# Kernel tuning notes

Measured on AMD Instinct MI355X. Metric: run time of the kernel, lower is better.

The kernel has to match this reference:

```python
import jax, jax.numpy as jnp
import numpy as np

B, T, V, E, H = 4096, 16, 512, 512, 1024


def setup_inputs() -> dict:
    key = jax.random.key(0)
    ks = jax.random.split(key, 8)
    s = 0.05  # weight init scale
    return {
        "encoded_input": jax.random.normal(ks[0], (B, H), jnp.float32),
        "target": jax.random.randint(ks[1], (B, T), 0, V, jnp.int32),
        "emb": jax.random.normal(ks[2], (V, E), jnp.float32) * s,
        "W_ih": jax.random.normal(ks[3], (4 * H, E), jnp.float32) * s,
        "W_hh": jax.random.normal(ks[4], (4 * H, H), jnp.float32) * s,
        "b_ih": jax.random.normal(ks[5], (4 * H,), jnp.float32) * s,
        "b_hh": jax.random.normal(ks[6], (4 * H,), jnp.float32) * s,
        "W_out": jax.random.normal(ks[7], (V, H), jnp.float32) * s,
    }


def reference(encoded_input, target, emb, W_ih, W_hh, b_ih, b_hh, W_out):
    # Teacher-forced char LSTM decoder. Dropout(0.1) is identity in eval mode.
    b, t = target.shape
    # input char ids: start token 0, then shifted targets
    inp_ids = jnp.concatenate(
        [jnp.zeros((b, 1), target.dtype), target[:, :-1]], axis=1)  # [B,T]
    x = emb[inp_ids]  # [B,T,E]
    # precompute input contribution to gates for all steps
    xg = jnp.einsum('bte,ge->btg', x, W_ih) + b_ih + b_hh  # [B,T,4H]

    def step(carry, xs):
        h, c = carry
        xg_t, tgt_t = xs  # [B,4H], [B]
        gates = xg_t + h @ W_hh.T  # [B,4H]
        i, f, g, o = jnp.split(gates, 4, axis=-1)  # torch order i,f,g,o
        i = jax.nn.sigmoid(i)
        f = jax.nn.sigmoid(f)
        g = jnp.tanh(g)
        o = jax.nn.sigmoid(o)
        c = f * c + i * g
        h = o * jnp.tanh(c)
        logits = h @ W_out.T  # [B,V]
        # NLL of log_softmax at target index, expressed stably
        lse = jax.nn.logsumexp(logits, axis=-1)
        tgt_logit = jnp.take_along_axis(logits, tgt_t[:, None], axis=1)[:, 0]
        loss_t = lse - tgt_logit  # [B]
        return (h, c), loss_t

    h0 = encoded_input  # hidden = (encoded, encoded) for 1 layer
    (_, _), losses = jax.lax.scan(
        step, (h0, h0),
        (jnp.swapaxes(xg, 0, 1), target.T))  # scan over time: [T,B,...]
    return losses.sum(axis=0) / t  # [B] per-example mean loss
```

## Files before the change

### kernel.cpp

```cpp
#include <hip/hip_runtime.h>
#include <hip/hip_bf16.h>
#include <stdint.h>

typedef __attribute__((ext_vector_type(8))) short bf16x8;
typedef __attribute__((ext_vector_type(4))) float f32x4;

#define DEV __device__ __forceinline__
#define MFMA16(a, b, c) __builtin_amdgcn_mfma_f32_16x16x32_bf16(a, b, c, 0, 0, 0)

static constexpr int Bn = 4096;
static constexpr int Tn = 16;
static constexpr int Vn = 512;
static constexpr int En = 512;
static constexpr int Hn = 1024;
static constexpr int G4 = 4096;

DEV unsigned short f2bf(float f) {
    union { float f; uint32_t u; } v; v.f = f;
    return (unsigned short)((v.u + 0x7fffu + ((v.u >> 16) & 1u)) >> 16);
}
DEV float bf2f(unsigned short h) {
    union { uint32_t u; float f; } v; v.u = (uint32_t)h << 16; return v.f;
}
DEV float sigmoidf_(float x) { return 1.f / (1.f + __expf(-x)); }
DEV float tanhf_(float x)    { return 1.f - 2.f / (1.f + __expf(2.f * x)); }

DEV bf16x8 cvt8(const float* p) {
    f32x4 a = *(const f32x4*)p;
    f32x4 b = *(const f32x4*)(p + 4);
    bf16x8 o;
    o[0] = (short)f2bf(a[0]); o[1] = (short)f2bf(a[1]);
    o[2] = (short)f2bf(a[2]); o[3] = (short)f2bf(a[3]);
    o[4] = (short)f2bf(b[0]); o[5] = (short)f2bf(b[1]);
    o[6] = (short)f2bf(b[2]); o[7] = (short)f2bf(b[3]);
    return o;
}

#define GLOAD16(s, d) __builtin_amdgcn_global_load_lds( \
    (const __attribute__((address_space(1))) uint32_t*)(s), \
    (__attribute__((address_space(3))) uint32_t*)(d), 16, 0, 0)

__launch_bounds__(1024, 4)
__global__ void lstm8(const unsigned short* __restrict__ Whp8,
                      const unsigned short* __restrict__ Hin,
                      const unsigned short* __restrict__ EGb,
                      const int* __restrict__ target, int t,
                      unsigned short* __restrict__ CstF,
                      unsigned short* __restrict__ Hout)
{
    __shared__ __align__(16) unsigned short lds[65536];

    const int tid = threadIdx.x;
    const int l   = tid & 63;
    const int w   = tid >> 6;
    const int wm  = w >> 2, wn = w & 3;
    const int q   = l >> 4, c15 = l & 15;
    const int bx  = blockIdx.x, by = blockIdx.y;
    const int n0  = bx * 256;
    const int U0  = by * 64;

    const int cBt = (((tid & 7) ^ ((tid >> 3) & 7)) << 3);
    const int sw0   = ((q ^ (c15 & 7)) << 3);
    const int offA0 = wm * 4096 + c15 * 64 + sw0;
    const int offB0 = wn * 4096 + c15 * 64 + sw0;

    f32x4 acc[4][4];
#pragma unroll
    for (int i = 0; i < 4; i++)
#pragma unroll
        for (int j = 0; j < 4; j++) acc[i][j] = f32x4{0.f, 0.f, 0.f, 0.f};

    auto stA = [&](int kts, int cbuf) {
        const unsigned short* page =
            Whp8 + (((size_t)(by * 16 + kts) * 2) << 13);
#pragma unroll
        for (int h = 0; h < 2; h++)
            GLOAD16(page + h * 8192 + tid * 8,
                    &lds[cbuf * 16384 + h * 8192 + tid * 8]);
    };
    auto stB = [&](int kts, int cbuf) {
#pragma unroll
        for (int h = 0; h < 2; h++)
            GLOAD16(Hin + (size_t)(n0 + h * 128 + (tid >> 3)) * Hn
                        + kts * 64 + cBt,
                    &lds[32768 + cbuf * 16384 + h * 8192 + tid * 8]);
    };

    stA(0, 0); stB(0, 0);
    stA(1, 1); stB(1, 1);
    asm volatile("s_waitcnt vmcnt(4)" ::: "memory");
    __builtin_amdgcn_s_barrier();

#pragma unroll 2
    for (int kt = 0; kt < 16; kt++) {
        const int cur = kt & 1;
        const unsigned short* Ab = &lds[cur * 16384];
        const unsigned short* Bb = &lds[32768 + cur * 16384];
        bf16x8 aF[4], bF[4];

#pragma unroll
        for (int i = 0; i < 4; i++)
            aF[i] = *(const bf16x8*)&Ab[offA0 + i * 1024];
#pragma unroll
        for (int j = 0; j < 4; j++)
            bF[j] = *(const bf16x8*)&Bb[offB0 + j * 1024];
        __builtin_amdgcn_s_setprio(1);
#pragma unroll
        for (int i = 0; i < 4; i++)
#pragma unroll
            for (int j = 0; j < 4; j++)
                acc[i][j] = MFMA16(aF[i], bF[j], acc[i][j]);
        __builtin_amdgcn_s_setprio(0);

#pragma unroll
        for (int i = 0; i < 4; i++)
            aF[i] = *(const bf16x8*)&Ab[(offA0 ^ 32) + i * 1024];
#pragma unroll
        for (int j = 0; j < 4; j++)
            bF[j] = *(const bf16x8*)&Bb[(offB0 ^ 32) + j * 1024];
        __builtin_amdgcn_s_setprio(1);
#pragma unroll
        for (int i = 0; i < 4; i++)
#pragma unroll
            for (int j = 0; j < 4; j++)
                acc[i][j] = MFMA16(aF[i], bF[j], acc[i][j]);
        __builtin_amdgcn_s_setprio(0);
        __builtin_amdgcn_s_barrier();

        const int kts = (kt + 2 < 16) ? (kt + 2) : 15;
        stA(kts, cur);
        stB(kts, cur);
        asm volatile("s_waitcnt vmcnt(4)" ::: "memory");
        __builtin_amdgcn_s_barrier();
    }

    int ids[4];
#pragma unroll
    for (int j = 0; j < 4; j++)
        ids[j] = (t > 0)
            ? target[(size_t)(n0 + wn * 64 + j * 16 + c15) * Tn + (t - 1)] : 0;

    unsigned short* sH = &lds[32768];
#pragma unroll
    for (int i = 0; i < 4; i++) {
        const int Uloc = wm * 16 + i * 4 + q;
#pragma unroll
        for (int j = 0; j < 4; j++) {
            uint2 egu = *(const uint2*)&EGb[(size_t)ids[j] * G4 + (U0 + Uloc) * 4];
            float e0 = bf2f((unsigned short)(egu.x & 0xffffu));
            float e1 = bf2f((unsigned short)(egu.x >> 16));
            float e2 = bf2f((unsigned short)(egu.y & 0xffffu));
            float e3 = bf2f((unsigned short)(egu.y >> 16));
            float ig = sigmoidf_(acc[i][j][0] + e0);
            float fg = sigmoidf_(acc[i][j][1] + e1);
            float gg = tanhf_  (acc[i][j][2] + e2);
            float og = sigmoidf_(acc[i][j][3] + e3);
            const size_t cidx =
                ((((size_t)(by * 16 + bx) * 16 + w) * 16 + i * 4 + j) << 6) + l;
            float cOld = bf2f(CstF[cidx]);
            float cNew = fg * cOld + ig * gg;
            float h    = og * tanhf_(cNew);
            CstF[cidx] = f2bf(cNew);
            const int bl = wn * 64 + j * 16 + c15;
            sH[bl * 64 + (Uloc ^ ((bl & 7) << 3))] = f2bf(h);
        }
    }
    __syncthreads();
    {
        const int row  = tid >> 2;
        const int part = tid & 3;
        size_t go = (size_t)(n0 + row) * Hn + U0;
#pragma unroll
        for (int s = 0; s < 2; s++) {
            const int slog = part * 2 + s;
            bf16x8 v = *(const bf16x8*)&sH[row * 64 + ((slog ^ (row & 7)) << 3)];
            *(bf16x8*)&Hout[go + slog * 8] = v;
        }
    }
}

__launch_bounds__(1024, 4)
__global__ void logits256(const unsigned short* __restrict__ A,
                          const unsigned short* __restrict__ Wob,
                          const int* __restrict__ target,
                          float* __restrict__ partS,
                          float* __restrict__ partT)
{
    __shared__ __align__(16) unsigned short lds[65536];
    __shared__ float redS[4 * 256];
    __shared__ float redT[4 * 256];
    __shared__ int   tgL[256];

    const int tid = threadIdx.x;
    const int l   = tid & 63;
    const int w   = tid >> 6;
    const int wm  = w >> 2, wn = w & 3;
    const int q   = l >> 4, c15 = l & 15;
    const int bid = blockIdx.x;
    const int rb  = bid & 255, cb = bid >> 8;
    const int r0  = rb * 256;
    const int v0  = cb * 256;

    if (tid < 256) {
        int ra = r0 + tid;
        tgL[tid] = target[(size_t)(ra & (Bn - 1)) * Tn + (ra >> 12)];
    }

    const int cBt = (((tid & 7) ^ ((tid >> 3) & 7)) << 3);
    const int sw0   = ((q ^ (c15 & 7)) << 3);
    const int offA0 = wm * 4096 + c15 * 64 + sw0;
    const int offB0 = wn * 4096 + c15 * 64 + sw0;

    f32x4 acc[4][4];
#pragma unroll
    for (int i = 0; i < 4; i++)
#pragma unroll
        for (int j = 0; j < 4; j++) acc[i][j] = f32x4{0.f, 0.f, 0.f, 0.f};

    auto stA = [&](int kts, int cbuf) {
#pragma unroll
        for (int h = 0; h < 2; h++)
            GLOAD16(A + (size_t)(r0 + h * 128 + (tid >> 3)) * Hn
                        + kts * 64 + cBt,
                    &lds[cbuf * 16384 + h * 8192 + tid * 8]);
    };
    auto stB = [&](int kts, int cbuf) {
#pragma unroll
        for (int h = 0; h < 2; h++)
            GLOAD16(Wob + (size_t)(v0 + h * 128 + (tid >> 3)) * Hn
                        + kts * 64 + cBt,
                    &lds[32768 + cbuf * 16384 + h * 8192 + tid * 8]);
    };

    stA(0, 0); stB(0, 0);
    stA(1, 1); stB(1, 1);
    asm volatile("s_waitcnt vmcnt(4)" ::: "memory");
    __builtin_amdgcn_s_barrier();

#pragma unroll 2
    for (int kt = 0; kt < 16; kt++) {
        const int cur = kt & 1;
        const unsigned short* Ab = &lds[cur * 16384];
        const unsigned short* Bb = &lds[32768 + cur * 16384];
        bf16x8 aF[4], bF[4];

#pragma unroll
        for (int i = 0; i < 4; i++)
            aF[i] = *(const bf16x8*)&Ab[offA0 + i * 1024];
#pragma unroll
        for (int j = 0; j < 4; j++)
            bF[j] = *(const bf16x8*)&Bb[offB0 + j * 1024];
        __builtin_amdgcn_s_setprio(1);
#pragma unroll
        for (int i = 0; i < 4; i++)
#pragma unroll
            for (int j = 0; j < 4; j++)
                acc[i][j] = MFMA16(aF[i], bF[j], acc[i][j]);
        __builtin_amdgcn_s_setprio(0);

#pragma unroll
        for (int i = 0; i < 4; i++)
            aF[i] = *(const bf16x8*)&Ab[(offA0 ^ 32) + i * 1024];
#pragma unroll
        for (int j = 0; j < 4; j++)
            bF[j] = *(const bf16x8*)&Bb[(offB0 ^ 32) + j * 1024];
        __builtin_amdgcn_s_setprio(1);
#pragma unroll
        for (int i = 0; i < 4; i++)
#pragma unroll
            for (int j = 0; j < 4; j++)
                acc[i][j] = MFMA16(aF[i], bF[j], acc[i][j]);
        __builtin_amdgcn_s_setprio(0);
        __builtin_amdgcn_s_barrier();

        const int kts = (kt + 2 < 16) ? (kt + 2) : 15;
        stA(kts, cur);
        stB(kts, cur);
        asm volatile("s_waitcnt vmcnt(4)" ::: "memory");
        __builtin_amdgcn_s_barrier();
    }

#pragma unroll
    for (int i = 0; i < 4; i++)
#pragma unroll
        for (int rr = 0; rr < 4; rr++) {
            const int rloc = wm * 64 + i * 16 + q * 4 + rr;
            const int tg = tgL[rloc];
            float ps = 0.f, tv = 0.f;
#pragma unroll
            for (int j = 0; j < 4; j++) {
                float v = acc[i][j][rr];
                ps += __expf(v);
                int col = v0 + wn * 64 + j * 16 + c15;
                tv += (col == tg) ? v : 0.f;
            }
#pragma unroll
            for (int d = 1; d < 16; d <<= 1) {
                ps += __shfl_xor(ps, d);
                tv += __shfl_xor(tv, d);
            }
            if (c15 == 0) {
                redS[wn * 256 + rloc] = ps;
                redT[wn * 256 + rloc] = tv;
            }
        }
    __syncthreads();
    if (tid < 256) {
        float se = 0.f, tv = 0.f;
#pragma unroll
        for (int k = 0; k < 4; k++) {
            se += redS[k * 256 + tid];
            tv += redT[k * 256 + tid];
        }
        partS[(size_t)cb * (Bn * Tn) + r0 + tid] = se;
        partT[(size_t)cb * (Bn * Tn) + r0 + tid] = tv;
    }
}

template <int BM, int BN, int EPI>
__launch_bounds__(256, 2)
__global__ void gemm_k(const unsigned short* __restrict__ A, int lda,
                       const unsigned short* __restrict__ Bw, int ldb,
                       int K,
                       const float* __restrict__ biasp,
                       float* __restrict__ Out,
                       unsigned short* __restrict__ Outb, int ldo)
{
    constexpr int BK = 32;
    constexpr int WM = BM / 2, WN = BN / 2;
    constexpr int MI = WM / 16, NJ = WN / 16;

    __shared__ __align__(16) unsigned short sA[BM * BK];
    __shared__ __align__(16) unsigned short sB[BN * BK];

    const int tid = threadIdx.x;
    const int l   = tid & 63;
    const int w   = tid >> 6;
    const int wm  = w >> 1, wn = w & 1;
    const int m0  = blockIdx.y * BM;
    const int n0  = blockIdx.x * BN;

    f32x4 acc[MI][NJ];
#pragma unroll
    for (int i = 0; i < MI; i++)
#pragma unroll
        for (int j = 0; j < NJ; j++) acc[i][j] = f32x4{0.f, 0.f, 0.f, 0.f};

    const int srow = l >> 2;
    const int scol = (l & 3) * 8;
    const int q    = l >> 4;
    const int c15  = l & 15;

    for (int k0 = 0; k0 < K; k0 += BK) {
#pragma unroll
        for (int c = 0; c < BM / 64; c++)
            GLOAD16(A + (size_t)(m0 + c * 64 + w * 16 + srow) * lda + k0 + scol,
                    &sA[(c * 64 + w * 16) * BK]);
#pragma unroll
        for (int c = 0; c < BN / 64; c++)
            GLOAD16(Bw + (size_t)(n0 + c * 64 + w * 16 + srow) * ldb + k0 + scol,
                    &sB[(c * 64 + w * 16) * BK]);
        __syncthreads();

        bf16x8 aF[MI], bF[NJ];
#pragma unroll
        for (int i = 0; i < MI; i++)
            aF[i] = *(const bf16x8*)&sA[(wm * WM + i * 16 + c15) * BK + q * 8];
#pragma unroll
        for (int j = 0; j < NJ; j++)
            bF[j] = *(const bf16x8*)&sB[(wn * WN + j * 16 + c15) * BK + q * 8];
#pragma unroll
        for (int i = 0; i < MI; i++)
#pragma unroll
            for (int j = 0; j < NJ; j++)
                acc[i][j] = MFMA16(aF[i], bF[j], acc[i][j]);
        __syncthreads();
    }

#pragma unroll
    for (int j = 0; j < NJ; j++) {
        const int colp = n0 + wn * WN + j * 16 + c15;
        const float bj = biasp ? biasp[colp] : 0.f;
#pragma unroll
        for (int i = 0; i < MI; i++) {
            const size_t rb = (size_t)(m0 + wm * WM + i * 16 + 4 * q);
#pragma unroll
            for (int r = 0; r < 4; r++) {
                float vv = acc[i][j][r] + bj;
                if constexpr (EPI == 0) Out[(rb + r) * ldo + colp] = vv;
                else Outb[(rb + r) * ldo + colp] = f2bf(vv);
            }
        }
    }
}

__global__ void prep_all(const float* __restrict__ Wih,
                         const float* __restrict__ Whh,
                         const float* __restrict__ bih,
                         const float* __restrict__ bhh,
                         const float* __restrict__ Wout,
                         const float* __restrict__ emb,
                         unsigned short* __restrict__ Wihp,
                         unsigned short* __restrict__ Whp8,
                         float* __restrict__ biasp,
                         unsigned short* __restrict__ Wob,
                         unsigned short* __restrict__ embb)
{
    const int b = blockIdx.x;
    if (b < 1024) {
        int i = b * 256 + threadIdx.x;
        int n = i >> 6, kc = (i & 63) * 8;
        int g = n & 3, u = n >> 2;
        *(bf16x8*)&Wihp[(size_t)n * En + kc] =
            cvt8(Wih + (size_t)(g * Hn + u) * En + kc);
    } else if (b < 3072) {
        int idx = (b - 1024) * 256 + threadIdx.x;
        int o = idx * 8;
        int p = o & 8191;
        int h = (o >> 13) & 1;
        int kt = (o >> 14) & 15;
        int by = o >> 18;
        int r = p >> 6;
        int slot = (p & 63) >> 3;
        int cl = ((slot ^ (r & 7)) << 3);
        int n = by * 256 + h * 128 + r;
        int g = n & 3, u = n >> 2;
        *(bf16x8*)&Whp8[o] =
            cvt8(Whh + (size_t)(g * Hn + u) * Hn + kt * 64 + cl);
    } else if (b < 3088) {
        int n = (b - 3072) * 256 + threadIdx.x;
        int g = n & 3, u = n >> 2;
        biasp[n] = bih[g * Hn + u] + bhh[g * Hn + u];
    } else if (b < 3344) {
        int i = (b - 3088) * 256 + threadIdx.x;
        size_t off = (size_t)i * 8;
        *(bf16x8*)&Wob[off] = cvt8(Wout + off);
    } else {
        int i = (b - 3344) * 256 + threadIdx.x;
        size_t off = (size_t)i * 8;
        *(bf16x8*)&embb[off] = cvt8(emb + off);
    }
}

__global__ void init_state(const float* __restrict__ enc,
                           unsigned short* __restrict__ CstF,
                           unsigned short* __restrict__ Xh0,
                           float* __restrict__ loss)
{
    int f = blockIdx.x * 256 + threadIdx.x;
    int l = f & 63, q = l >> 4, c15 = l & 15;
    int ij = (f >> 6) & 15, i = ij >> 2, j = ij & 3;
    int w = (f >> 10) & 15, wm = w >> 2, wn = w & 3;
    int bx = (f >> 14) & 15, by = (f >> 18) & 15;
    int b = bx * 256 + wn * 64 + j * 16 + c15;
    int U = by * 64 + wm * 16 + i * 4 + q;
    CstF[f] = f2bf(enc[(size_t)b * Hn + U]);
    if (f < Bn * Hn / 8) {
        int m = f >> 7, u8 = (f & 127) * 8;
        *(bf16x8*)&Xh0[(size_t)m * Hn + u8] = cvt8(enc + (size_t)m * Hn + u8);
    }
    if (f < Bn) loss[f] = 0.f;
}

__global__ void lse_k(const unsigned short* __restrict__ lg,
                      const int* __restrict__ target, int t,
                      float* __restrict__ lossOut)
{
    int w = threadIdx.x >> 6, l = threadIdx.x & 63;
    int ra = blockIdx.x * 4 + w;
    const unsigned short* row = lg + (size_t)ra * Vn;
    bf16x8 v = *(const bf16x8*)&row[l * 8];
    float x0 = bf2f((unsigned short)v[0]), x1 = bf2f((unsigned short)v[1]);
    float x2 = bf2f((unsigned short)v[2]), x3 = bf2f((unsigned short)v[3]);
    float x4 = bf2f((unsigned short)v[4]), x5 = bf2f((unsigned short)v[5]);
    float x6 = bf2f((unsigned short)v[6]), x7 = bf2f((unsigned short)v[7]);
    float mx = fmaxf(fmaxf(fmaxf(x0, x1), fmaxf(x2, x3)),
                     fmaxf(fmaxf(x4, x5), fmaxf(x6, x7)));
#pragma unroll
    for (int d = 1; d < 64; d <<= 1) mx = fmaxf(mx, __shfl_xor(mx, d));
    float se = __expf(x0 - mx) + __expf(x1 - mx) + __expf(x2 - mx) +
               __expf(x3 - mx) + __expf(x4 - mx) + __expf(x5 - mx) +
               __expf(x6 - mx) + __expf(x7 - mx);
#pragma unroll
    for (int d = 1; d < 64; d <<= 1) se += __shfl_xor(se, d);
    if (l == 0) {
        int tg = target[(size_t)ra * Tn + t];
        lossOut[ra] += (mx + __logf(se)) - bf2f(row[tg]);
    }
}

__global__ void finalize_p(const float* __restrict__ partS,
                           const float* __restrict__ partT,
                           float* __restrict__ out)
{
    int m = blockIdx.x * 256 + threadIdx.x;
    float s = 0.f;
#pragma unroll
    for (int k = 0; k < 16; k++) {
        size_t ra = (size_t)k * Bn + m;
        float se = partS[ra] + partS[(size_t)(Bn * Tn) + ra];
        float tv = partT[ra] + partT[(size_t)(Bn * Tn) + ra];
        s += __logf(se) - tv;
    }
    out[m] = s * (1.f / 16.f);
}

__global__ void finalize_s(const float* __restrict__ loss,
                           float* __restrict__ out)
{
    int m = blockIdx.x * 256 + threadIdx.x;
    out[m] = loss[m] * (1.f / 16.f);
}

extern "C" void kernel_launch(void* const* d_in, const int* in_sizes, int n_in,
                              void* d_out, int out_size, void* d_ws, size_t ws_size,
                              hipStream_t stream)
{
    const float* enc    = (const float*)d_in[0];
    const int*   target = (const int*)d_in[1];
    const float* emb    = (const float*)d_in[2];
    const float* Wih    = (const float*)d_in[3];
    const float* Whh    = (const float*)d_in[4];
    const float* bih    = (const float*)d_in[5];
    const float* bhh    = (const float*)d_in[6];
    const float* Wout   = (const float*)d_in[7];
    float* out = (float*)d_out;
    (void)in_sizes; (void)n_in; (void)out_size;

    constexpr size_t SZ_Wihp  = (size_t)G4 * En * 2;
    constexpr size_t SZ_Whp8  = (size_t)G4 * Hn * 2;
    constexpr size_t SZ_Wob   = (size_t)Vn * Hn * 2;
    constexpr size_t SZ_biasp = (size_t)G4 * 4;
    constexpr size_t SZ_embb  = (size_t)Vn * En * 2;
    constexpr size_t SZ_EGb   = (size_t)Vn * G4 * 2;
    constexpr size_t SZ_Cst   = (size_t)Bn * Hn * 2;
    constexpr size_t SZ_H     = (size_t)Bn * Hn * 2;
    constexpr size_t SZ_LGS   = (size_t)Bn * Vn * 2;
    constexpr size_t SZ_PART  = (size_t)2 * Bn * Tn * 4;
    auto pad = [](size_t b) { return (b + 255) & ~(size_t)255; };
    const size_t fixed = pad(SZ_Wihp) + pad(SZ_Whp8) + pad(SZ_Wob) +
                         pad(SZ_biasp) + pad(SZ_embb) + pad(SZ_EGb) +
                         pad(SZ_Cst);
    const size_t needB = fixed + 17 * pad(SZ_H) + pad(SZ_LGS) +
                         2 * pad(SZ_PART);
    const bool batched = ws_size >= needB;

    size_t off = 0;
    char* base = (char*)d_ws;
    auto alloc = [&](size_t bytes) -> void* {
        void* p = base + off; off += pad(bytes); return p;
    };
    unsigned short* Wihp  = (unsigned short*)alloc(SZ_Wihp);
    unsigned short* Whp8  = (unsigned short*)alloc(SZ_Whp8);
    unsigned short* Wob   = (unsigned short*)alloc(SZ_Wob);
    float*          biasp = (float*)alloc(SZ_biasp);
    unsigned short* embb  = (unsigned short*)alloc(SZ_embb);
    unsigned short* EGb   = (unsigned short*)alloc(SZ_EGb);
    unsigned short* CstF  = (unsigned short*)alloc(SZ_Cst);
    const int nslot = batched ? 17 : 3;
    unsigned short* Hs    = (unsigned short*)alloc((size_t)nslot * pad(SZ_H));
    unsigned short* lgS   = (unsigned short*)alloc(SZ_LGS);
    float*          partS = (float*)alloc(SZ_PART);
    float*          partT = (float*)alloc(SZ_PART);
    const size_t HSLOT = pad(SZ_H) / 2;

    prep_all  <<<3472, 256, 0, stream>>>(Wih, Whh, bih, bhh, Wout, emb,
                                         Wihp, Whp8, biasp, Wob, embb);
    init_state<<<16384, 256, 0, stream>>>(enc, CstF, Hs, partS);

    gemm_k<128, 128, 2><<<dim3(32, 4), 256, 0, stream>>>(
        embb, En, Wihp, En, En, biasp, nullptr, EGb, G4);

    if (batched) {
        for (int t = 0; t < Tn; t++)
            lstm8<<<dim3(16, 16), 1024, 0, stream>>>(
                Whp8, Hs + (size_t)t * HSLOT, EGb, target, t, CstF,
                Hs + (size_t)(t + 1) * HSLOT);
        logits256<<<512, 1024, 0, stream>>>(
            Hs + HSLOT, Wob, target, partS, partT);
        finalize_p<<<16, 256, 0, stream>>>(partS, partT, out);
    } else {
        for (int t = 0; t < Tn; t++) {
            unsigned short* hIn  = Hs + (size_t)(t % 3) * HSLOT;
            unsigned short* hOut = Hs + (size_t)((t + 1) % 3) * HSLOT;
            lstm8<<<dim3(16, 16), 1024, 0, stream>>>(
                Whp8, hIn, EGb, target, t, CstF, hOut);
            gemm_k<128, 64, 2><<<dim3(8, 32), 256, 0, stream>>>(
                hOut, Hn, Wob, Hn, Hn, nullptr, nullptr, lgS, Vn);
            lse_k<<<1024, 256, 0, stream>>>(lgS, target, t, partS);
        }
        finalize_s<<<16, 256, 0, stream>>>(partS, out);
    }
}
```

Measured before the change: 835.1 us.

## Cover full vocab per logits block and fold init_state into prep_all

The batched logits kernel now gives each block 128 rows across all 512 vocab columns (8 column waves) with BK=32, rather than 256x256 tiles split across two column blocks. The per-row log-sum-exp and target logit are finished inside the block, so there are no partial sums to write and the finalize step only sums per-step losses. The state initialization kernel is merged into the weight-prep kernel to save a launch. In exchange the A tile is smaller, each K step has a shallower MFMA chain, and each block reloads all of W_out.

```diff
diff --git a/kernel.cpp b/kernel.cpp
--- a/kernel.cpp
+++ b/kernel.cpp
@@ -180,36 +180,36 @@
 }
 
 __launch_bounds__(1024, 4)
-__global__ void logits256(const unsigned short* __restrict__ A,
+__global__ void logits512(const unsigned short* __restrict__ A,
                           const unsigned short* __restrict__ Wob,
                           const int* __restrict__ target,
-                          float* __restrict__ partS,
-                          float* __restrict__ partT)
-{
-    __shared__ __align__(16) unsigned short lds[65536];
-    __shared__ float redS[4 * 256];
-    __shared__ float redT[4 * 256];
-    __shared__ int   tgL[256];
+                          float* __restrict__ lossT)
+{
+    __shared__ __align__(16) unsigned short lds[40960];
+    __shared__ float redS[8 * 128];
+    __shared__ float redT[8 * 128];
+    __shared__ int   tgL[128];
 
     const int tid = threadIdx.x;
     const int l   = tid & 63;
     const int w   = tid >> 6;
-    const int wm  = w >> 2, wn = w & 3;
+    const int wm  = w >> 3, wn = w & 7;
     const int q   = l >> 4, c15 = l & 15;
-    const int bid = blockIdx.x;
-    const int rb  = bid & 255, cb = bid >> 8;
-    const int r0  = rb * 256;
-    const int v0  = cb * 256;
-
-    if (tid < 256) {
+    const int r0  = blockIdx.x * 128;
+
+    if (tid < 128) {
         int ra = r0 + tid;
         tgL[tid] = target[(size_t)(ra & (Bn - 1)) * Tn + (ra >> 12)];
     }
 
-    const int cBt = (((tid & 7) ^ ((tid >> 3) & 7)) << 3);
-    const int sw0   = ((q ^ (c15 & 7)) << 3);
-    const int offA0 = wm * 4096 + c15 * 64 + sw0;
-    const int offB0 = wn * 4096 + c15 * 64 + sw0;
+    const int tA   = tid & 511;
+    const int rowA = tA >> 2;
+    const int colA = (((tA & 3) ^ (rowA & 3)) << 3);
+    const int rowB = tid >> 2;
+    const int colB = (((tid & 3) ^ (rowB & 3)) << 3);
+    const int swz  = ((q ^ (c15 & 3)) << 3);
+    const int offA = (wm * 64 + c15) * 32 + swz;
+    const int offB = (wn * 64 + c15) * 32 + swz;
 
     f32x4 acc[4][4];
 #pragma unroll
@@ -217,53 +217,33 @@
 #pragma unroll
         for (int j = 0; j < 4; j++) acc[i][j] = f32x4{0.f, 0.f, 0.f, 0.f};
 
-    auto stA = [&](int kts, int cbuf) {
-#pragma unroll
-        for (int h = 0; h < 2; h++)
-            GLOAD16(A + (size_t)(r0 + h * 128 + (tid >> 3)) * Hn
-                        + kts * 64 + cBt,
-                    &lds[cbuf * 16384 + h * 8192 + tid * 8]);
+    auto stage = [&](int kts, int cbuf) {
+        GLOAD16(A + (size_t)(r0 + rowA) * Hn + kts * 32 + colA,
+                &lds[cbuf * 4096 + tA * 8]);
+#pragma unroll
+        for (int R = 0; R < 2; R++)
+            GLOAD16(Wob + (size_t)(R * 256 + rowB) * Hn + kts * 32 + colB,
+                    &lds[8192 + cbuf * 16384 + R * 8192 + tid * 8]);
     };
-    auto stB = [&](int kts, int cbuf) {
-#pragma unroll
-        for (int h = 0; h < 2; h++)
-            GLOAD16(Wob + (size_t)(v0 + h * 128 + (tid >> 3)) * Hn
-                        + kts * 64 + cBt,
-                    &lds[32768 + cbuf * 16384 + h * 8192 + tid * 8]);
-    };
-
-    stA(0, 0); stB(0, 0);
-    stA(1, 1); stB(1, 1);
-    asm volatile("s_waitcnt vmcnt(4)" ::: "memory");
+
+    stage(0, 0);
+    stage(1, 1);
+    asm volatile("s_waitcnt vmcnt(3)" ::: "memory");
     __builtin_amdgcn_s_barrier();
 
 #pragma unroll 2
-    for (int kt = 0; kt < 16; kt++) {
+    for (int kt = 0; kt < 32; kt++) {
         const int cur = kt & 1;
-        const unsigned short* Ab = &lds[cur * 16384];
-        const unsigned short* Bb = &lds[32768 + cur * 16384];
+        const unsigned short* Ab = &lds[cur * 4096];
+        const unsigned short* Bb = &lds[8192 + cur * 16384];
         bf16x8 aF[4], bF[4];
 
 #pragma unroll
         for (int i = 0; i < 4; i++)
-            aF[i] = *(const bf16x8*)&Ab[offA0 + i * 1024];
+            aF[i] = *(const bf16x8*)&Ab[offA + i * 512];
 #pragma unroll
         for (int j = 0; j < 4; j++)
-            bF[j] = *(const bf16x8*)&Bb[offB0 + j * 1024];
-        __builtin_amdgcn_s_setprio(1);
-#pragma unroll
-        for (int i = 0; i < 4; i++)
-#pragma unroll
-            for (int j = 0; j < 4; j++)
-                acc[i][j] = MFMA16(aF[i], bF[j], acc[i][j]);
-        __builtin_amdgcn_s_setprio(0);
-
-#pragma unroll
-        for (int i = 0; i < 4; i++)
-            aF[i] = *(const bf16x8*)&Ab[(offA0 ^ 32) + i * 1024];
-#pragma unroll
-        for (int j = 0; j < 4; j++)
-            bF[j] = *(const bf16x8*)&Bb[(offB0 ^ 32) + j * 1024];
+            bF[j] = *(const bf16x8*)&Bb[offB + j * 512];
         __builtin_amdgcn_s_setprio(1);
 #pragma unroll
         for (int i = 0; i < 4; i++)
@@ -273,10 +253,9 @@
         __builtin_amdgcn_s_setprio(0);
         __builtin_amdgcn_s_barrier();
 
-        const int kts = (kt + 2 < 16) ? (kt + 2) : 15;
-        stA(kts, cur);
-        stB(kts, cur);
-        asm volatile("s_waitcnt vmcnt(4)" ::: "memory");
+        const int kts = (kt + 2 < 32) ? (kt + 2) : 31;
+        stage(kts, cur);
+        asm volatile("s_waitcnt vmcnt(3)" ::: "memory");
         __builtin_amdgcn_s_barrier();
     }
 
@@ -291,7 +270,7 @@
             for (int j = 0; j < 4; j++) {
                 float v = acc[i][j][rr];
                 ps += __expf(v);
-                int col = v0 + wn * 64 + j * 16 + c15;
+                int col = wn * 64 + j * 16 + c15;
                 tv += (col == tg) ? v : 0.f;
             }
 #pragma unroll
@@ -300,20 +279,19 @@
                 tv += __shfl_xor(tv, d);
             }
             if (c15 == 0) {
-                redS[wn * 256 + rloc] = ps;
-                redT[wn * 256 + rloc] = tv;
+                redS[wn * 128 + rloc] = ps;
+                redT[wn * 128 + rloc] = tv;
             }
         }
     __syncthreads();
-    if (tid < 256) {
+    if (tid < 128) {
         float se = 0.f, tv = 0.f;
 #pragma unroll
-        for (int k = 0; k < 4; k++) {
-            se += redS[k * 256 + tid];
-            tv += redT[k * 256 + tid];
-        }
-        partS[(size_t)cb * (Bn * Tn) + r0 + tid] = se;
-        partT[(size_t)cb * (Bn * Tn) + r0 + tid] = tv;
+        for (int k = 0; k < 8; k++) {
+            se += redS[k * 128 + tid];
+            tv += redT[k * 128 + tid];
+        }
+        lossT[r0 + tid] = __logf(se) - tv;
     }
 }
 
@@ -400,11 +378,15 @@
                          const float* __restrict__ bhh,
                          const float* __restrict__ Wout,
                          const float* __restrict__ emb,
+                         const float* __restrict__ enc,
                          unsigned short* __restrict__ Wihp,
                          unsigned short* __restrict__ Whp8,
                          float* __restrict__ biasp,
                          unsigned short* __restrict__ Wob,
-                         unsigned short* __restrict__ embb)
+                         unsigned short* __restrict__ embb,
+                         unsigned short* __restrict__ CstF,
+                         unsigned short* __restrict__ Xh0,
+                         float* __restrict__ loss)
 {
     const int b = blockIdx.x;
     if (b < 1024) {
@@ -435,31 +417,26 @@
         int i = (b - 3088) * 256 + threadIdx.x;
         size_t off = (size_t)i * 8;
         *(bf16x8*)&Wob[off] = cvt8(Wout + off);
-    } else {
+    } else if (b < 3472) {
         int i = (b - 3344) * 256 + threadIdx.x;
         size_t off = (size_t)i * 8;
         *(bf16x8*)&embb[off] = cvt8(emb + off);
-    }
-}
-
-__global__ void init_state(const float* __restrict__ enc,
-                           unsigned short* __restrict__ CstF,
-                           unsigned short* __restrict__ Xh0,
-                           float* __restrict__ loss)
-{
-    int f = blockIdx.x * 256 + threadIdx.x;
-    int l = f & 63, q = l >> 4, c15 = l & 15;
-    int ij = (f >> 6) & 15, i = ij >> 2, j = ij & 3;
-    int w = (f >> 10) & 15, wm = w >> 2, wn = w & 3;
-    int bx = (f >> 14) & 15, by = (f >> 18) & 15;
-    int b = bx * 256 + wn * 64 + j * 16 + c15;
-    int U = by * 64 + wm * 16 + i * 4 + q;
-    CstF[f] = f2bf(enc[(size_t)b * Hn + U]);
-    if (f < Bn * Hn / 8) {
-        int m = f >> 7, u8 = (f & 127) * 8;
-        *(bf16x8*)&Xh0[(size_t)m * Hn + u8] = cvt8(enc + (size_t)m * Hn + u8);
-    }
-    if (f < Bn) loss[f] = 0.f;
+    } else {
+        int f = (b - 3472) * 256 + threadIdx.x;
+        int l = f & 63, q = l >> 4, c15 = l & 15;
+        int ij = (f >> 6) & 15, i = ij >> 2, j = ij & 3;
+        int w = (f >> 10) & 15, wm = w >> 2, wn = w & 3;
+        int bx = (f >> 14) & 15, by = (f >> 18) & 15;
+        int bb = bx * 256 + wn * 64 + j * 16 + c15;
+        int U  = by * 64 + wm * 16 + i * 4 + q;
+        CstF[f] = f2bf(enc[(size_t)bb * Hn + U]);
+        if (f < Bn * Hn / 8) {
+            int m = f >> 7, u8 = (f & 127) * 8;
+            *(bf16x8*)&Xh0[(size_t)m * Hn + u8] =
+                cvt8(enc + (size_t)m * Hn + u8);
+        }
+        if (f < Bn) loss[f] = 0.f;
+    }
 }
 
 __global__ void lse_k(const unsigned short* __restrict__ lg,
@@ -489,19 +466,13 @@
     }
 }
 
-__global__ void finalize_p(const float* __restrict__ partS,
-                           const float* __restrict__ partT,
+__global__ void finalize_b(const float* __restrict__ lossT,
                            float* __restrict__ out)
 {
     int m = blockIdx.x * 256 + threadIdx.x;
     float s = 0.f;
 #pragma unroll
-    for (int k = 0; k < 16; k++) {
-        size_t ra = (size_t)k * Bn + m;
-        float se = partS[ra] + partS[(size_t)(Bn * Tn) + ra];
-        float tv = partT[ra] + partT[(size_t)(Bn * Tn) + ra];
-        s += __logf(se) - tv;
-    }
+    for (int k = 0; k < 16; k++) s += lossT[(size_t)k * Bn + m];
     out[m] = s * (1.f / 16.f);
 }
 
@@ -536,13 +507,12 @@
     constexpr size_t SZ_Cst   = (size_t)Bn * Hn * 2;
     constexpr size_t SZ_H     = (size_t)Bn * Hn * 2;
     constexpr size_t SZ_LGS   = (size_t)Bn * Vn * 2;
-    constexpr size_t SZ_PART  = (size_t)2 * Bn * Tn * 4;
+    constexpr size_t SZ_LT    = (size_t)Bn * Tn * 4;
     auto pad = [](size_t b) { return (b + 255) & ~(size_t)255; };
     const size_t fixed = pad(SZ_Wihp) + pad(SZ_Whp8) + pad(SZ_Wob) +
                          pad(SZ_biasp) + pad(SZ_embb) + pad(SZ_EGb) +
                          pad(SZ_Cst);
-    const size_t needB = fixed + 17 * pad(SZ_H) + pad(SZ_LGS) +
-                         2 * pad(SZ_PART);
+    const size_t needB = fixed + 17 * pad(SZ_H) + pad(SZ_LGS) + pad(SZ_LT);
     const bool batched = ws_size >= needB;
 
     size_t off = 0;
@@ -560,13 +530,12 @@
     const int nslot = batched ? 17 : 3;
     unsigned short* Hs    = (unsigned short*)alloc((size_t)nslot * pad(SZ_H));
     unsigned short* lgS   = (unsigned short*)alloc(SZ_LGS);
-    float*          partS = (float*)alloc(SZ_PART);
-    float*          partT = (float*)alloc(SZ_PART);
+    float*          lossT = (float*)alloc(SZ_LT);
     const size_t HSLOT = pad(SZ_H) / 2;
 
-    prep_all  <<<3472, 256, 0, stream>>>(Wih, Whh, bih, bhh, Wout, emb,
-                                         Wihp, Whp8, biasp, Wob, embb);
-    init_state<<<16384, 256, 0, stream>>>(enc, CstF, Hs, partS);
+    prep_all<<<19856, 256, 0, stream>>>(Wih, Whh, bih, bhh, Wout, emb, enc,
+                                        Wihp, Whp8, biasp, Wob, embb,
+                                        CstF, Hs, lossT);
 
     gemm_k<128, 128, 2><<<dim3(32, 4), 256, 0, stream>>>(
         embb, En, Wihp, En, En, biasp, nullptr, EGb, G4);
@@ -576,9 +545,9 @@
             lstm8<<<dim3(16, 16), 1024, 0, stream>>>(
                 Whp8, Hs + (size_t)t * HSLOT, EGb, target, t, CstF,
                 Hs + (size_t)(t + 1) * HSLOT);
-        logits256<<<512, 1024, 0, stream>>>(
-            Hs + HSLOT, Wob, target, partS, partT);
-        finalize_p<<<16, 256, 0, stream>>>(partS, partT, out);
+        logits512<<<512, 1024, 0, stream>>>(
+            Hs + HSLOT, Wob, target, lossT);
+        finalize_b<<<16, 256, 0, stream>>>(lossT, out);
     } else {
         for (int t = 0; t < Tn; t++) {
             unsigned short* hIn  = Hs + (size_t)(t % 3) * HSLOT;
@@ -587,8 +556,8 @@
                 Whp8, hIn, EGb, target, t, CstF, hOut);
             gemm_k<128, 64, 2><<<dim3(8, 32), 256, 0, stream>>>(
                 hOut, Hn, Wob, Hn, Hn, nullptr, nullptr, lgS, Vn);
-            lse_k<<<1024, 256, 0, stream>>>(lgS, target, t, partS);
-        }
-        finalize_s<<<16, 256, 0, stream>>>(partS, out);
-    }
-}
+            lse_k<<<1024, 256, 0, stream>>>(lgS, target, t, lossT);
+        }
+        finalize_s<<<16, 256, 0, stream>>>(lossT, out);
+    }
+}
```

New measurement: 844.7 us. No clear change (+1.1%).
